# Kernel tuning notes

Hardware: AMD Instinct MI355X
Metric: run time of the kernel (lower is better)

The kernel has to match this reference:

```python
import jax, jax.numpy as jnp
import numpy as np

N, E, D, R = 100000, 1600000, 64, 16


def setup_inputs() -> dict:
    key = jax.random.key(0)
    k = jax.random.split(key, 8)
    feat = jax.random.normal(k[0], (N, D), dtype=jnp.float32)
    # xavier-uniform-ish scale (gain=sqrt(2), fan_in=fan_out=D) ~ std 0.177
    relation_weight = jax.random.normal(k[1], (R, D, D), dtype=jnp.float32) * 0.17
    relation_embed = jax.random.normal(k[2], (R, D), dtype=jnp.float32)
    W1 = jax.random.normal(k[3], (D, D), dtype=jnp.float32) * 0.1
    W2 = jax.random.normal(k[4], (D, D), dtype=jnp.float32) * 0.1
    src = jax.random.randint(k[5], (E,), 0, N, dtype=jnp.int32)
    dst = jax.random.randint(k[6], (E,), 0, N, dtype=jnp.int32)
    etype = jax.random.randint(k[7], (E,), 0, R, dtype=jnp.int32)
    return {"feat": feat, "relation_weight": relation_weight,
            "relation_embed": relation_embed, "W1": W1, "W2": W2,
            "src": src, "dst": dst, "etype": etype}


def reference(feat, relation_weight, relation_embed, W1, W2, src, dst, etype):
    n = feat.shape[0]
    # Project every node through every relation once ([N,R,D]) instead of
    # materializing the per-edge [E,D,D] weight gather; same math as
    # t_r = h_src @ W_{r(e)}, h_r = h_dst @ W_{r(e)}.
    proj = jnp.einsum('nd,rdo->nro', feat, relation_weight)  # [N,R,D]
    t_r = proj[src, etype]                                   # [E,D]
    h_r = proj[dst, etype]                                   # [E,D]
    # attention logit per edge: <t_r, tanh(h_r + r_embed)>
    att = jnp.sum(t_r * jnp.tanh(h_r + relation_embed[etype]), axis=-1)  # [E]
    # edge softmax over incoming edges of each destination node
    seg_max = jax.ops.segment_max(att, dst, num_segments=n)
    e = jnp.exp(att - seg_max[dst])
    seg_sum = jax.ops.segment_sum(e, dst, num_segments=n)
    a = e / seg_sum[dst]                                     # [E]
    # weighted aggregation of source features
    msgs = feat[src] * a[:, None]                            # [E,D]
    h_nb = jax.ops.segment_sum(msgs, dst, num_segments=n)    # [N,D]
    # Bi-interaction residual (torch leaky_relu default slope 0.01)
    out = (jax.nn.leaky_relu((feat + h_nb) @ W1.T, negative_slope=0.01)
           + jax.nn.leaky_relu((feat * h_nb) @ W2.T, negative_slope=0.01))
    return out
```

## Files before the change

kernel.cpp:

```cpp
#include <hip/hip_runtime.h>
#include <math.h>

#define D 64

typedef __attribute__((ext_vector_type(8))) short bf16x8;
typedef __attribute__((ext_vector_type(4))) float f32x4;

static __device__ __forceinline__ unsigned short f2bf(float f) {
    unsigned int u = __float_as_uint(f);
    unsigned int r = (u + 0x7FFFu + ((u >> 16) & 1u)) >> 16;
    return (unsigned short)r;
}
static __device__ __forceinline__ float bf2f(unsigned short h) {
    return __uint_as_float(((unsigned int)h) << 16);
}

#if defined(__has_builtin)
#if __has_builtin(__builtin_amdgcn_cvt_pk_bf16_f32)
#define HAVE_PK_BF16 1
#endif
#endif

static __device__ __forceinline__ unsigned int pk2bf(float a, float b) {
#ifdef HAVE_PK_BF16
    auto v = __builtin_amdgcn_cvt_pk_bf16_f32(a, b);
    return *(unsigned int*)&v;
#else
    return (unsigned int)f2bf(a) | ((unsigned int)f2bf(b) << 16);
#endif
}

static __device__ __forceinline__ float fast_tanh(float x) {
    float e = __expf(2.f * x);
    float r = __builtin_amdgcn_rcpf(e + 1.f);
    return 1.f - 2.f * r;
}

typedef __attribute__((address_space(1))) const unsigned int as1_uint;
typedef __attribute__((address_space(3))) unsigned int as3_uint;
static __device__ __forceinline__ void dma16(const void* g, void* l) {
    __builtin_amdgcn_global_load_lds((as1_uint*)g, (as3_uint*)l, 16, 0, 0);
}

__global__ __launch_bounds__(256) void k_wsplit(const float* __restrict__ W,
                                                unsigned short* __restrict__ B1h,
                                                unsigned short* __restrict__ B1l,
                                                unsigned short* __restrict__ B2h,
                                                unsigned short* __restrict__ B2l,
                                                int R) {
    int idx = blockIdx.x * 256 + threadIdx.x;
    int per_g = R * 512;
    if (idx >= 2 * per_g) return;
    int g = idx / per_g;
    int rest = idx % per_g;
    int r = rest >> 9;
    int rest2 = rest & 511;
    int c = rest2 >> 7;
    int kb = (rest2 >> 6) & 1;
    int lane = rest2 & 63;
    int m = lane & 15, q = lane >> 4;
    bf16x8 hv, lv;
    #pragma unroll
    for (int j = 0; j < 8; ++j) {
        float v;
        if (g == 0) v = W[(size_t)r * 4096 + (kb * 32 + q * 8 + j) * 64 + (c * 16 + m)];
        else        v = W[(size_t)r * 4096 + (c * 16 + m) * 64 + (kb * 32 + q * 8 + j)];
        unsigned short h = f2bf(v);
        hv[j] = (short)h;
        lv[j] = (short)f2bf(v - bf2f(h));
    }
    size_t off = ((((size_t)r * 4 + c) * 2 + kb) * 64 + lane) * 8;
    unsigned short* ph = (g == 0) ? B1h : B2h;
    unsigned short* pl = (g == 0) ? B1l : B2l;
    *(bf16x8*)&ph[off] = hv;
    *(bf16x8*)&pl[off] = lv;
}

__global__ __launch_bounds__(256) void k_wsplit2(const float* __restrict__ W1,
                                                 const float* __restrict__ W2,
                                                 unsigned short* __restrict__ F1h,
                                                 unsigned short* __restrict__ F1l,
                                                 unsigned short* __restrict__ F2h,
                                                 unsigned short* __restrict__ F2l) {
    int idx = blockIdx.x * 256 + threadIdx.x;
    if (idx >= 1024) return;
    int g = idx >> 9;
    int rest2 = idx & 511;
    int c = rest2 >> 7;
    int kb = (rest2 >> 6) & 1;
    int lane = rest2 & 63;
    int m = lane & 15, q = lane >> 4;
    const float* W = g ? W2 : W1;
    bf16x8 hv, lv;
    #pragma unroll
    for (int j = 0; j < 8; ++j) {
        float v = W[(c * 16 + m) * 64 + kb * 32 + q * 8 + j];
        unsigned short h = f2bf(v);
        hv[j] = (short)h;
        lv[j] = (short)f2bf(v - bf2f(h));
    }
    size_t off = (((size_t)c * 2 + kb) * 64 + lane) * 8;
    unsigned short* ph = g ? F2h : F1h;
    unsigned short* pl = g ? F2l : F1l;
    *(bf16x8*)&ph[off] = hv;
    *(bf16x8*)&pl[off] = lv;
}

#define NB3 256

__global__ __launch_bounds__(256) void k_bcount(const int* __restrict__ dst,
                                                int* __restrict__ cnt,
                                                int E, int CH, int NBUK) {
    __shared__ int h[1024];
    const int t = threadIdx.x, blk = blockIdx.x;
    for (int b = t; b < NBUK; b += 256) h[b] = 0;
    __syncthreads();
    const int s0 = blk * CH, s1 = min(E, s0 + CH);
    for (int e = s0 + t; e < s1; e += 256)
        atomicAdd(&h[dst[e] >> 7], 1);
    __syncthreads();
    for (int b = t; b < NBUK; b += 256)
        cnt[(b << 8) | blk] = h[b];
}

__global__ __launch_bounds__(256) void k_bscatter(const int* __restrict__ src,
                                                  const int* __restrict__ dst,
                                                  const int* __restrict__ etype,
                                                  const int* __restrict__ csc,
                                                  int* __restrict__ ebuf,
                                                  int E, int CH, int NBUK) {
    __shared__ int cur[1024];
    const int t = threadIdx.x, blk = blockIdx.x;
    for (int b = t; b < NBUK; b += 256) cur[b] = csc[(b << 8) | blk];
    __syncthreads();
    const int s0 = blk * CH, s1 = min(E, s0 + CH);
    for (int e = s0 + t; e < s1; e += 256) {
        int d = dst[e];
        int b = d >> 7;
        int pos = atomicAdd(&cur[b], 1);
        unsigned int pk = (unsigned int)src[e] | ((unsigned int)etype[e] << 20)
                        | ((unsigned int)(d & 127) << 25);
        ebuf[pos] = (int)pk;
    }
}

__global__ __launch_bounds__(256) void k_bcsr(const int* __restrict__ ebuf,
                                              const int* __restrict__ csc,
                                              int* __restrict__ offsets,
                                              int* __restrict__ spack,
                                              int N, int E, int NBUK) {
    __shared__ int sdeg[128], sincl[128], scur[128];
    const int t = threadIdx.x, b = blockIdx.x;
    const int s0 = csc[b << 8];
    const int s1 = csc[(b + 1) << 8];
    if (t < 128) { sdeg[t] = 0; }
    __syncthreads();
    for (int e = s0 + t; e < s1; e += 256)
        atomicAdd(&sdeg[((unsigned int)ebuf[e]) >> 25], 1);
    __syncthreads();
    if (t < 128) sincl[t] = sdeg[t];
    __syncthreads();
    for (int off = 1; off < 128; off <<= 1) {
        int v = 0;
        if (t < 128 && t >= off) v = sincl[t - off];
        __syncthreads();
        if (t < 128) sincl[t] += v;
        __syncthreads();
    }
    if (t < 128) {
        int excl = sincl[t] - sdeg[t];
        scur[t] = s0 + excl;
        int n = (b << 7) + t;
        if (n < N) offsets[n] = s0 + excl;
    }
    if (b == NBUK - 1 && t == 0) offsets[N] = E;
    __syncthreads();
    for (int e = s0 + t; e < s1; e += 256) {
        unsigned int pk = (unsigned int)ebuf[e];
        int i = pk >> 25;
        int p = atomicAdd(&scur[i], 1);
        spack[p] = (int)(pk & 0x01FFFFFFu);
    }
}

__global__ __launch_bounds__(1024) void k_scan1(const int* __restrict__ deg, int* __restrict__ tscan,
                                                int* __restrict__ bsum, int N) {
    __shared__ int s[1024];
    const int t = threadIdx.x;
    const int i = blockIdx.x * 1024 + t;
    int v = (i < N) ? deg[i] : 0;
    s[t] = v;
    __syncthreads();
    for (int off = 1; off < 1024; off <<= 1) {
        int tmp = (t >= off) ? s[t - off] : 0;
        __syncthreads();
        s[t] += tmp;
        __syncthreads();
    }
    if (i < N) tscan[i] = s[t];
    if (t == 1023) bsum[blockIdx.x] = s[1023];
}

__global__ __launch_bounds__(1024) void k_scan2(const int* __restrict__ bsum, int* __restrict__ bofs, int NB) {
    __shared__ int s[1024];
    const int t = threadIdx.x;
    int carry = 0;
    for (int b0 = 0; b0 < NB; b0 += 1024) {
        int i = b0 + t;
        int v = (i < NB) ? bsum[i] : 0;
        s[t] = v;
        __syncthreads();
        for (int off = 1; off < 1024; off <<= 1) {
            int tmp = (t >= off) ? s[t - off] : 0;
            __syncthreads();
            s[t] += tmp;
            __syncthreads();
        }
        if (i < NB) bofs[i] = carry + s[t] - v;
        int tot = s[1023];
        __syncthreads();
        carry += tot;
    }
}

__global__ __launch_bounds__(256) void k_scanout(const int* __restrict__ tscan, const int* __restrict__ bofs,
                                                 int* __restrict__ outv, int L) {
    int i = blockIdx.x * 256 + threadIdx.x;
    if (i <= L) {
        outv[i] = (i == 0) ? 0 : (tscan[i - 1] + bofs[(i - 1) >> 10]);
    }
}

__global__ __launch_bounds__(256, 4) void k_projv(const float* __restrict__ feat,
                                                  const unsigned short* __restrict__ B1h,
                                                  const unsigned short* __restrict__ B1l,
                                                  const unsigned short* __restrict__ B2h,
                                                  const unsigned short* __restrict__ B2l,
                                                  const float* __restrict__ emb,
                                                  unsigned short* __restrict__ V,
                                                  int N, int R, int nrq) {
    const int tile = blockIdx.x / nrq;
    const int rq   = blockIdx.x % nrq;
    const int rbase = rq * 4;
    const int rcnt  = (R - rbase < 4) ? (R - rbase) : 4;
    const int n0 = tile * 128;
    __shared__ __align__(16) unsigned short Bbuf[32][512];
    __shared__ __align__(16) unsigned short Us[4][1024];
    const int t = threadIdx.x;
    const int lane = t & 63, w = t >> 6;
    const int m = lane & 15, q = lane >> 4;

    bf16x8 ah[2][2], al[2][2];
    #pragma unroll
    for (int s = 0; s < 2; ++s) {
        int n = n0 + w * 32 + s * 16 + m;
        const float* rowp = feat + (size_t)n * D;
        #pragma unroll
        for (int kb = 0; kb < 2; ++kb) {
            int d0 = kb * 32 + q * 8;
            float4 v0 = make_float4(0.f, 0.f, 0.f, 0.f), v1 = v0;
            if (n < N) { v0 = *(const float4*)(rowp + d0); v1 = *(const float4*)(rowp + d0 + 4); }
            float vals[8] = {v0.x, v0.y, v0.z, v0.w, v1.x, v1.y, v1.z, v1.w};
            bf16x8 hv, lv;
            #pragma unroll
            for (int j = 0; j < 8; ++j) {
                unsigned short h = f2bf(vals[j]);
                hv[j] = (short)h;
                lv[j] = (short)f2bf(vals[j] - bf2f(h));
            }
            ah[s][kb] = hv; al[s][kb] = lv;
        }
    }

    auto stage_half = [&](int r, int half) {
        const unsigned short* arr = half ? ((w < 2) ? B2h : B2l)
                                         : ((w < 2) ? B1h : B1l);
        const unsigned short* gp = arr + (size_t)r * 4096 + (size_t)(w & 1) * 2048 + lane * 8;
        unsigned short* lp = &Bbuf[half * 16 + (w >> 1) * 8 + (w & 1) * 4][0];
        #pragma unroll
        for (int i = 0; i < 4; ++i)
            dma16(gp + i * 512, lp + i * 512);
    };

    stage_half(rbase, 0);
    stage_half(rbase, 1);
    __syncthreads();

    for (int rr = 0; rr < rcnt; ++rr) {
        const int r = rbase + rr;
        float em[4];
        #pragma unroll
        for (int c = 0; c < 4; ++c) em[c] = emb[r * 64 + c * 16 + m];

        f32x4 acc[4][2];
        #pragma unroll
        for (int c = 0; c < 4; ++c)
            #pragma unroll
            for (int s = 0; s < 2; ++s) acc[c][s] = (f32x4){0.f, 0.f, 0.f, 0.f};
        #pragma unroll
        for (int c = 0; c < 4; ++c) {
            bf16x8 bh[2], bl[2];
            #pragma unroll
            for (int kb = 0; kb < 2; ++kb) {
                bh[kb] = *(const bf16x8*)&Bbuf[c * 2 + kb][lane * 8];
                bl[kb] = *(const bf16x8*)&Bbuf[8 + c * 2 + kb][lane * 8];
            }
            #pragma unroll
            for (int s = 0; s < 2; ++s)
                #pragma unroll
                for (int kb = 0; kb < 2; ++kb) {
                    acc[c][s] = __builtin_amdgcn_mfma_f32_16x16x32_bf16(ah[s][kb], bh[kb], acc[c][s], 0, 0, 0);
                    acc[c][s] = __builtin_amdgcn_mfma_f32_16x16x32_bf16(al[s][kb], bh[kb], acc[c][s], 0, 0, 0);
                    acc[c][s] = __builtin_amdgcn_mfma_f32_16x16x32_bf16(ah[s][kb], bl[kb], acc[c][s], 0, 0, 0);
                }
        }

        __syncthreads();
        if (rr + 1 < rcnt) stage_half(r + 1, 0);

        #pragma unroll
        for (int s = 0; s < 2; ++s) {
            #pragma unroll
            for (int c = 0; c < 4; ++c) {
                int o = c * 16 + m;
                int kb2 = o >> 5;
                int q2 = (o >> 3) & 3;
                int j = o & 7;
                int Fb = kb2 * 64 + q2 * 16 + q * 4;
                #pragma unroll
                for (int i = 0; i < 4; i += 2) {
                    float t0 = fast_tanh(acc[c][s][i] + em[c]);
                    float t1 = fast_tanh(acc[c][s][i + 1] + em[c]);
                    unsigned int pk = pk2bf(t0, t1);
                    Us[w][((Fb + i) ^ q2) * 8 + j]     = (unsigned short)(pk & 0xFFFF);
                    Us[w][((Fb + i + 1) ^ q2) * 8 + j] = (unsigned short)(pk >> 16);
                }
            }

            bf16x8 ua[2];
            #pragma unroll
            for (int kb = 0; kb < 2; ++kb) {
                int F = kb * 64 + lane;
                ua[kb] = *(const bf16x8*)&Us[w][(F ^ (lane >> 4)) * 8];
            }
            f32x4 acc2[4];
            #pragma unroll
            for (int c = 0; c < 4; ++c) acc2[c] = (f32x4){0.f, 0.f, 0.f, 0.f};
            #pragma unroll
            for (int c = 0; c < 4; ++c) {
                bf16x8 bh[2], bl[2];
                #pragma unroll
                for (int kb = 0; kb < 2; ++kb) {
                    bh[kb] = *(const bf16x8*)&Bbuf[16 + c * 2 + kb][lane * 8];
                    bl[kb] = *(const bf16x8*)&Bbuf[24 + c * 2 + kb][lane * 8];
                }
                #pragma unroll
                for (int kb = 0; kb < 2; ++kb) {
                    acc2[c] = __builtin_amdgcn_mfma_f32_16x16x32_bf16(ua[kb], bh[kb], acc2[c], 0, 0, 0);
                    acc2[c] = __builtin_amdgcn_mfma_f32_16x16x32_bf16(ua[kb], bl[kb], acc2[c], 0, 0, 0);
                }
            }

            #pragma unroll
            for (int i = 0; i < 4; ++i) {
                int n = n0 + w * 32 + s * 16 + q * 4 + i;
                if (n < N) {
                    uint2 pv;
                    pv.x = pk2bf(acc2[0][i], acc2[1][i]);
                    pv.y = pk2bf(acc2[2][i], acc2[3][i]);
                    *(uint2*)&V[((size_t)n * R + r) * 64 + m * 4] = pv;
                }
            }
        }

        __syncthreads();
        if (rr + 1 < rcnt) stage_half(r + 1, 1);
    }
}

__global__ __launch_bounds__(256) void k_fused2(const unsigned short* __restrict__ V,
                                                const float* __restrict__ feat,
                                                const int* __restrict__ offsets,
                                                const int* __restrict__ spack,
                                                float* __restrict__ h_nb,
                                                int N, int R) {
    const int lane = threadIdx.x & 63;
    const int wav  = threadIdx.x >> 6;
    const int g    = lane >> 4;
    const int k    = lane & 15;
    const int n = blockIdx.x * 4 + wav;
    __shared__ float vlds[4][1024];
    if (n >= N) return;

    const unsigned int* v32 = (const unsigned int*)(V + (size_t)n * R * D);
    #pragma unroll
    for (int j = 0; j < 8; ++j) {
        int uidx = j * 64 + lane;
        unsigned int u = v32[uidx];
        int r  = uidx >> 5;
        int k2 = uidx & 31;
        int mm = k2 >> 1;
        int cc = (k2 & 1) * 2;
        int o  = cc * 16 + mm;
        vlds[wav][r * 64 + o]      = bf2f((unsigned short)(u & 0xFFFF));
        vlds[wav][r * 64 + o + 16] = bf2f((unsigned short)(u >> 16));
    }

    const int beg = offsets[n], end = offsets[n + 1];
    float m = -INFINITY, l = 0.f;
    float4 acc = make_float4(0.f, 0.f, 0.f, 0.f);

    if (beg < end) {
        int e = beg + g;
        bool ok = e < end;
        int pk = spack[ok ? e : (end - 1)];
        float4 f = *(const float4*)&feat[(size_t)(pk & 0xFFFFF) * D + k * 4];

        for (int i = beg; i < end; i += 4) {
            const int   et  = pk >> 20;
            const float4 fc = f;
            const bool  okc = ok;
            int e2 = i + 4 + g;
            ok = e2 < end;
            pk = spack[ok ? e2 : (end - 1)];
            f = *(const float4*)&feat[(size_t)(pk & 0xFFFFF) * D + k * 4];

            float4 v = *(const float4*)&vlds[wav][et * 64 + k * 4];
            float p = fc.x * v.x + fc.y * v.y + fc.z * v.z + fc.w * v.w;
            p += __shfl_xor(p, 1, 64);
            p += __shfl_xor(p, 2, 64);
            p += __shfl_xor(p, 4, 64);
            p += __shfl_xor(p, 8, 64);
            p = okc ? p : -INFINITY;
            float tmx = fmaxf(p, __shfl_xor(p, 16, 64));
            float nm4 = fmaxf(tmx, __shfl_xor(tmx, 32, 64));
            float nm  = fmaxf(m, nm4);
            float scale = __expf(m - nm);
            float wg    = __expf(p - nm);
            float sw = wg + __shfl_xor(wg, 16, 64);
            sw += __shfl_xor(sw, 32, 64);
            l = l * scale + sw;
            acc.x = acc.x * scale + wg * fc.x;
            acc.y = acc.y * scale + wg * fc.y;
            acc.z = acc.z * scale + wg * fc.z;
            acc.w = acc.w * scale + wg * fc.w;
            m = nm;
        }
        acc.x += __shfl_xor(acc.x, 16, 64);
        acc.y += __shfl_xor(acc.y, 16, 64);
        acc.z += __shfl_xor(acc.z, 16, 64);
        acc.w += __shfl_xor(acc.w, 16, 64);
        acc.x += __shfl_xor(acc.x, 32, 64);
        acc.y += __shfl_xor(acc.y, 32, 64);
        acc.z += __shfl_xor(acc.z, 32, 64);
        acc.w += __shfl_xor(acc.w, 32, 64);
        float inv = 1.f / l;
        acc.x *= inv; acc.y *= inv; acc.z *= inv; acc.w *= inv;
    }
    if (lane < 16)
        *(float4*)&h_nb[(size_t)n * D + k * 4] = acc;
}

__global__ __launch_bounds__(256, 2) void k_final(const float* __restrict__ feat,
                                                  const float* __restrict__ h_nb,
                                                  const unsigned short* __restrict__ F1h,
                                                  const unsigned short* __restrict__ F1l,
                                                  const unsigned short* __restrict__ F2h,
                                                  const unsigned short* __restrict__ F2l,
                                                  float* __restrict__ out, int N) {
    const int n0 = blockIdx.x * 128;
    __shared__ __align__(16) unsigned short Wlds[4][4096];
    const int t = threadIdx.x;
    const int lane = t & 63, w = t >> 6;
    const int m = lane & 15, q = lane >> 4;

    const unsigned short* warr = (w == 0) ? F1h : (w == 1) ? F1l : (w == 2) ? F2h : F2l;
    #pragma unroll
    for (int i = 0; i < 8; ++i)
        dma16(warr + i * 512 + lane * 8, &Wlds[w][i * 512]);

    bf16x8 sh[2][2], sl[2][2], ph[2][2], pl[2][2];
    #pragma unroll
    for (int s = 0; s < 2; ++s) {
        int n = n0 + w * 32 + s * 16 + m;
        const float* fp = feat + (size_t)n * D;
        const float* hp = h_nb + (size_t)n * D;
        #pragma unroll
        for (int kb = 0; kb < 2; ++kb) {
            int d0 = kb * 32 + q * 8;
            float4 f0 = make_float4(0.f, 0.f, 0.f, 0.f), f1 = f0, h0 = f0, h1 = f0;
            if (n < N) {
                f0 = *(const float4*)(fp + d0); f1 = *(const float4*)(fp + d0 + 4);
                h0 = *(const float4*)(hp + d0); h1 = *(const float4*)(hp + d0 + 4);
            }
            float fv[8] = {f0.x, f0.y, f0.z, f0.w, f1.x, f1.y, f1.z, f1.w};
            float hv[8] = {h0.x, h0.y, h0.z, h0.w, h1.x, h1.y, h1.z, h1.w};
            bf16x8 a, b, c2, d2;
            #pragma unroll
            for (int j = 0; j < 8; ++j) {
                float xs = fv[j] + hv[j];
                float xp = fv[j] * hv[j];
                unsigned short hs = f2bf(xs);
                unsigned short hp2 = f2bf(xp);
                a[j]  = (short)hs;
                b[j]  = (short)f2bf(xs - bf2f(hs));
                c2[j] = (short)hp2;
                d2[j] = (short)f2bf(xp - bf2f(hp2));
            }
            sh[s][kb] = a; sl[s][kb] = b; ph[s][kb] = c2; pl[s][kb] = d2;
        }
    }
    __syncthreads();

    f32x4 a1[4][2], a2[4][2];
    #pragma unroll
    for (int c = 0; c < 4; ++c)
        #pragma unroll
        for (int s = 0; s < 2; ++s) {
            a1[c][s] = (f32x4){0.f, 0.f, 0.f, 0.f};
            a2[c][s] = (f32x4){0.f, 0.f, 0.f, 0.f};
        }
    #pragma unroll
    for (int c = 0; c < 4; ++c) {
        bf16x8 b1h[2], b1l[2], b2h[2], b2l[2];
        #pragma unroll
        for (int kb = 0; kb < 2; ++kb) {
            int o = (c * 2 + kb) * 512 + lane * 8;
            b1h[kb] = *(const bf16x8*)&Wlds[0][o];
            b1l[kb] = *(const bf16x8*)&Wlds[1][o];
            b2h[kb] = *(const bf16x8*)&Wlds[2][o];
            b2l[kb] = *(const bf16x8*)&Wlds[3][o];
        }
        #pragma unroll
        for (int kb = 0; kb < 2; ++kb)
            #pragma unroll
            for (int s = 0; s < 2; ++s) {
                a1[c][s] = __builtin_amdgcn_mfma_f32_16x16x32_bf16(sh[s][kb], b1h[kb], a1[c][s], 0, 0, 0);
                a1[c][s] = __builtin_amdgcn_mfma_f32_16x16x32_bf16(sl[s][kb], b1h[kb], a1[c][s], 0, 0, 0);
                a1[c][s] = __builtin_amdgcn_mfma_f32_16x16x32_bf16(sh[s][kb], b1l[kb], a1[c][s], 0, 0, 0);
                a2[c][s] = __builtin_amdgcn_mfma_f32_16x16x32_bf16(ph[s][kb], b2h[kb], a2[c][s], 0, 0, 0);
                a2[c][s] = __builtin_amdgcn_mfma_f32_16x16x32_bf16(pl[s][kb], b2h[kb], a2[c][s], 0, 0, 0);
                a2[c][s] = __builtin_amdgcn_mfma_f32_16x16x32_bf16(ph[s][kb], b2l[kb], a2[c][s], 0, 0, 0);
            }
    }

    #pragma unroll
    for (int s = 0; s < 2; ++s)
        #pragma unroll
        for (int i = 0; i < 4; ++i) {
            int n = n0 + w * 32 + s * 16 + q * 4 + i;
            if (n < N) {
                #pragma unroll
                for (int c = 0; c < 4; ++c) {
                    float o1 = a1[c][s][i];
                    float o2 = a2[c][s][i];
                    o1 = (o1 > 0.f) ? o1 : 0.01f * o1;
                    o2 = (o2 > 0.f) ? o2 : 0.01f * o2;
                    out[(size_t)n * D + c * 16 + m] = o1 + o2;
                }
            }
        }
}

extern "C" void kernel_launch(void* const* d_in, const int* in_sizes, int n_in,
                              void* d_out, int out_size, void* d_ws, size_t ws_size,
                              hipStream_t stream) {
    const float* feat  = (const float*)d_in[0];
    const float* relW  = (const float*)d_in[1];
    const float* relE  = (const float*)d_in[2];
    const float* W1    = (const float*)d_in[3];
    const float* W2    = (const float*)d_in[4];
    const int*   src   = (const int*)d_in[5];
    const int*   dst   = (const int*)d_in[6];
    const int*   etype = (const int*)d_in[7];
    float* out = (float*)d_out;

    const int N = in_sizes[0] / D;
    const int R = in_sizes[2] / D;
    const int E = in_sizes[5];

    char* w = (char*)d_ws;
    size_t off = 0;
    auto alloc = [&](size_t bytes) -> void* {
        void* p = w + off;
        off = (off + bytes + 255) & ~(size_t)255;
        return p;
    };
    unsigned short* varr = (unsigned short*)alloc((size_t)N * R * D * sizeof(unsigned short));
    float* h_nb   = (float*)alloc((size_t)N * D * sizeof(float));
    int* offsets  = (int*)alloc((size_t)(N + 1) * sizeof(int));
    int* bsum     = (int*)alloc(2048 * sizeof(int));
    int* bofs     = (int*)alloc(2048 * sizeof(int));
    int* spack    = (int*)alloc((size_t)E * sizeof(int));
    size_t wfrag = (size_t)R * 4 * 2 * 64 * 8;
    unsigned short* B1h = (unsigned short*)alloc(wfrag * sizeof(unsigned short));
    unsigned short* B1l = (unsigned short*)alloc(wfrag * sizeof(unsigned short));
    unsigned short* B2h = (unsigned short*)alloc(wfrag * sizeof(unsigned short));
    unsigned short* B2l = (unsigned short*)alloc(wfrag * sizeof(unsigned short));
    unsigned short* F1h = (unsigned short*)alloc(4096 * sizeof(unsigned short));
    unsigned short* F1l = (unsigned short*)alloc(4096 * sizeof(unsigned short));
    unsigned short* F2h = (unsigned short*)alloc(4096 * sizeof(unsigned short));
    unsigned short* F2l = (unsigned short*)alloc(4096 * sizeof(unsigned short));
    (void)ws_size; (void)n_in; (void)out_size;

    const int NBUK = (N + 127) >> 7;
    const int CH   = (E + NB3 - 1) / NB3;
    const int L    = NBUK << 8;
    int* ebuf = (int*)varr;
    int* cnt  = ebuf + E;
    int* tsc  = cnt + L;
    int* csc  = tsc + L;
    const int NBscan = (L + 1023) / 1024;

    const int nrq = (R + 3) / 4;
    const int ntiles = (N + 127) / 128;

    k_wsplit<<<(2 * R * 512 + 255) / 256, 256, 0, stream>>>(relW, B1h, B1l, B2h, B2l, R);
    k_wsplit2<<<4, 256, 0, stream>>>(W1, W2, F1h, F1l, F2h, F2l);
    k_bcount<<<NB3, 256, 0, stream>>>(dst, cnt, E, CH, NBUK);
    k_scan1<<<NBscan, 1024, 0, stream>>>(cnt, tsc, bsum, L);
    k_scan2<<<1, 1024, 0, stream>>>(bsum, bofs, NBscan);
    k_scanout<<<(L + 1 + 255) / 256, 256, 0, stream>>>(tsc, bofs, csc, L);
    k_bscatter<<<NB3, 256, 0, stream>>>(src, dst, etype, csc, ebuf, E, CH, NBUK);
    k_bcsr<<<NBUK, 256, 0, stream>>>(ebuf, csc, offsets, spack, N, E, NBUK);
    k_projv<<<ntiles * nrq, 256, 0, stream>>>(feat, B1h, B1l, B2h, B2l, relE, varr, N, R, nrq);
    k_fused2<<<(N + 3) / 4, 256, 0, stream>>>(varr, feat, offsets, spack, h_nb, N, R);
    k_final<<<(N + 127) / 128, 256, 0, stream>>>(feat, h_nb, F1h, F1l, F2h, F2l, out, N);
}
```

Baseline: 369.1 us.

## Gather fp16 source features in edge kernel and merge small setup kernels

Adds a kernel that casts node features to fp16 once, and makes the fused edge kernel gather 8-byte fp16 rows instead of 16-byte fp32 rows. This halves the random-gather traffic over 1.6M edges. The two weight-split kernels are merged into one launch, and the scan-output kernel is removed: consumers now compute the exclusive-scan value inline from the tile scan and block offsets. The trade-offs are an extra pass over the features to cast them and fp16 rounding in the attention logits and messages.

```diff
diff --git a/kernel.cpp b/kernel.cpp
--- a/kernel.cpp
+++ b/kernel.cpp
@@ -42,68 +42,88 @@
     __builtin_amdgcn_global_load_lds((as1_uint*)g, (as3_uint*)l, 16, 0, 0);
 }
 
-__global__ __launch_bounds__(256) void k_wsplit(const float* __restrict__ W,
-                                                unsigned short* __restrict__ B1h,
-                                                unsigned short* __restrict__ B1l,
-                                                unsigned short* __restrict__ B2h,
-                                                unsigned short* __restrict__ B2l,
-                                                int R) {
-    int idx = blockIdx.x * 256 + threadIdx.x;
-    int per_g = R * 512;
-    if (idx >= 2 * per_g) return;
-    int g = idx / per_g;
-    int rest = idx % per_g;
-    int r = rest >> 9;
-    int rest2 = rest & 511;
-    int c = rest2 >> 7;
-    int kb = (rest2 >> 6) & 1;
-    int lane = rest2 & 63;
-    int m = lane & 15, q = lane >> 4;
-    bf16x8 hv, lv;
-    #pragma unroll
-    for (int j = 0; j < 8; ++j) {
-        float v;
-        if (g == 0) v = W[(size_t)r * 4096 + (kb * 32 + q * 8 + j) * 64 + (c * 16 + m)];
-        else        v = W[(size_t)r * 4096 + (c * 16 + m) * 64 + (kb * 32 + q * 8 + j)];
-        unsigned short h = f2bf(v);
-        hv[j] = (short)h;
-        lv[j] = (short)f2bf(v - bf2f(h));
-    }
-    size_t off = ((((size_t)r * 4 + c) * 2 + kb) * 64 + lane) * 8;
-    unsigned short* ph = (g == 0) ? B1h : B2h;
-    unsigned short* pl = (g == 0) ? B1l : B2l;
-    *(bf16x8*)&ph[off] = hv;
-    *(bf16x8*)&pl[off] = lv;
-}
-
-__global__ __launch_bounds__(256) void k_wsplit2(const float* __restrict__ W1,
+static __device__ __forceinline__ int exscan_at(const int* __restrict__ tsc,
+                                                const int* __restrict__ bofs, int i) {
+    return (i == 0) ? 0 : (tsc[i - 1] + bofs[(i - 1) >> 10]);
+}
+
+__global__ __launch_bounds__(256) void k_wsplitA(const float* __restrict__ W,
+                                                 unsigned short* __restrict__ B1h,
+                                                 unsigned short* __restrict__ B1l,
+                                                 unsigned short* __restrict__ B2h,
+                                                 unsigned short* __restrict__ B2l,
+                                                 const float* __restrict__ W1,
                                                  const float* __restrict__ W2,
                                                  unsigned short* __restrict__ F1h,
                                                  unsigned short* __restrict__ F1l,
                                                  unsigned short* __restrict__ F2h,
-                                                 unsigned short* __restrict__ F2l) {
+                                                 unsigned short* __restrict__ F2l,
+                                                 int R) {
     int idx = blockIdx.x * 256 + threadIdx.x;
-    if (idx >= 1024) return;
-    int g = idx >> 9;
-    int rest2 = idx & 511;
-    int c = rest2 >> 7;
-    int kb = (rest2 >> 6) & 1;
-    int lane = rest2 & 63;
-    int m = lane & 15, q = lane >> 4;
-    const float* W = g ? W2 : W1;
-    bf16x8 hv, lv;
-    #pragma unroll
-    for (int j = 0; j < 8; ++j) {
-        float v = W[(c * 16 + m) * 64 + kb * 32 + q * 8 + j];
-        unsigned short h = f2bf(v);
-        hv[j] = (short)h;
-        lv[j] = (short)f2bf(v - bf2f(h));
-    }
-    size_t off = (((size_t)c * 2 + kb) * 64 + lane) * 8;
-    unsigned short* ph = g ? F2h : F1h;
-    unsigned short* pl = g ? F2l : F1l;
-    *(bf16x8*)&ph[off] = hv;
-    *(bf16x8*)&pl[off] = lv;
+    int per_g = R * 512;
+    if (idx < 2 * per_g) {
+        int g = idx / per_g;
+        int rest = idx % per_g;
+        int r = rest >> 9;
+        int rest2 = rest & 511;
+        int c = rest2 >> 7;
+        int kb = (rest2 >> 6) & 1;
+        int lane = rest2 & 63;
+        int m = lane & 15, q = lane >> 4;
+        bf16x8 hv, lv;
+        #pragma unroll
+        for (int j = 0; j < 8; ++j) {
+            float v;
+            if (g == 0) v = W[(size_t)r * 4096 + (kb * 32 + q * 8 + j) * 64 + (c * 16 + m)];
+            else        v = W[(size_t)r * 4096 + (c * 16 + m) * 64 + (kb * 32 + q * 8 + j)];
+            unsigned short h = f2bf(v);
+            hv[j] = (short)h;
+            lv[j] = (short)f2bf(v - bf2f(h));
+        }
+        size_t off = ((((size_t)r * 4 + c) * 2 + kb) * 64 + lane) * 8;
+        unsigned short* ph = (g == 0) ? B1h : B2h;
+        unsigned short* pl = (g == 0) ? B1l : B2l;
+        *(bf16x8*)&ph[off] = hv;
+        *(bf16x8*)&pl[off] = lv;
+    } else {
+        int idx2 = idx - 2 * per_g;
+        if (idx2 >= 1024) return;
+        int g = idx2 >> 9;
+        int rest2 = idx2 & 511;
+        int c = rest2 >> 7;
+        int kb = (rest2 >> 6) & 1;
+        int lane = rest2 & 63;
+        int m = lane & 15, q = lane >> 4;
+        const float* Wx = g ? W2 : W1;
+        bf16x8 hv, lv;
+        #pragma unroll
+        for (int j = 0; j < 8; ++j) {
+            float v = Wx[(c * 16 + m) * 64 + kb * 32 + q * 8 + j];
+            unsigned short h = f2bf(v);
+            hv[j] = (short)h;
+            lv[j] = (short)f2bf(v - bf2f(h));
+        }
+        size_t off = (((size_t)c * 2 + kb) * 64 + lane) * 8;
+        unsigned short* ph = g ? F2h : F1h;
+        unsigned short* pl = g ? F2l : F1l;
+        *(bf16x8*)&ph[off] = hv;
+        *(bf16x8*)&pl[off] = lv;
+    }
+}
+
+__global__ __launch_bounds__(256) void k_fcast(const float* __restrict__ feat,
+                                               unsigned short* __restrict__ fb,
+                                               int total4) {
+    int i = blockIdx.x * 256 + threadIdx.x;
+    if (i < total4) {
+        float4 v = ((const float4*)feat)[i];
+        union { _Float16 h[4]; uint2 u; } cv;
+        cv.h[0] = (_Float16)v.x;
+        cv.h[1] = (_Float16)v.y;
+        cv.h[2] = (_Float16)v.z;
+        cv.h[3] = (_Float16)v.w;
+        ((uint2*)fb)[i] = cv.u;
+    }
 }
 
 #define NB3 256
@@ -126,12 +146,13 @@
 __global__ __launch_bounds__(256) void k_bscatter(const int* __restrict__ src,
                                                   const int* __restrict__ dst,
                                                   const int* __restrict__ etype,
-                                                  const int* __restrict__ csc,
+                                                  const int* __restrict__ tsc,
+                                                  const int* __restrict__ bofs,
                                                   int* __restrict__ ebuf,
                                                   int E, int CH, int NBUK) {
     __shared__ int cur[1024];
     const int t = threadIdx.x, blk = blockIdx.x;
-    for (int b = t; b < NBUK; b += 256) cur[b] = csc[(b << 8) | blk];
+    for (int b = t; b < NBUK; b += 256) cur[b] = exscan_at(tsc, bofs, (b << 8) | blk);
     __syncthreads();
     const int s0 = blk * CH, s1 = min(E, s0 + CH);
     for (int e = s0 + t; e < s1; e += 256) {
@@ -145,14 +166,15 @@
 }
 
 __global__ __launch_bounds__(256) void k_bcsr(const int* __restrict__ ebuf,
-                                              const int* __restrict__ csc,
+                                              const int* __restrict__ tsc,
+                                              const int* __restrict__ bofs,
                                               int* __restrict__ offsets,
                                               int* __restrict__ spack,
                                               int N, int E, int NBUK) {
     __shared__ int sdeg[128], sincl[128], scur[128];
     const int t = threadIdx.x, b = blockIdx.x;
-    const int s0 = csc[b << 8];
-    const int s1 = csc[(b + 1) << 8];
+    const int s0 = exscan_at(tsc, bofs, b << 8);
+    const int s1 = exscan_at(tsc, bofs, (b + 1) << 8);
     if (t < 128) { sdeg[t] = 0; }
     __syncthreads();
     for (int e = s0 + t; e < s1; e += 256)
@@ -220,14 +242,6 @@
         int tot = s[1023];
         __syncthreads();
         carry += tot;
-    }
-}
-
-__global__ __launch_bounds__(256) void k_scanout(const int* __restrict__ tscan, const int* __restrict__ bofs,
-                                                 int* __restrict__ outv, int L) {
-    int i = blockIdx.x * 256 + threadIdx.x;
-    if (i <= L) {
-        outv[i] = (i == 0) ? 0 : (tscan[i - 1] + bofs[(i - 1) >> 10]);
     }
 }
 
@@ -379,7 +393,7 @@
 }
 
 __global__ __launch_bounds__(256) void k_fused2(const unsigned short* __restrict__ V,
-                                                const float* __restrict__ feat,
+                                                const unsigned short* __restrict__ fb,
                                                 const int* __restrict__ offsets,
                                                 const int* __restrict__ spack,
                                                 float* __restrict__ h_nb,
@@ -414,16 +428,24 @@
         int e = beg + g;
         bool ok = e < end;
         int pk = spack[ok ? e : (end - 1)];
-        float4 f = *(const float4*)&feat[(size_t)(pk & 0xFFFFF) * D + k * 4];
+        uint2 fv = *(const uint2*)&fb[(size_t)(pk & 0xFFFFF) * D + k * 4];
 
         for (int i = beg; i < end; i += 4) {
             const int   et  = pk >> 20;
-            const float4 fc = f;
+            const uint2 fvc = fv;
             const bool  okc = ok;
             int e2 = i + 4 + g;
             ok = e2 < end;
             pk = spack[ok ? e2 : (end - 1)];
-            f = *(const float4*)&feat[(size_t)(pk & 0xFFFFF) * D + k * 4];
+            fv = *(const uint2*)&fb[(size_t)(pk & 0xFFFFF) * D + k * 4];
+
+            union { uint2 u; _Float16 h[4]; } cv;
+            cv.u = fvc;
+            float4 fc;
+            fc.x = (float)cv.h[0];
+            fc.y = (float)cv.h[1];
+            fc.z = (float)cv.h[2];
+            fc.w = (float)cv.h[3];
 
             float4 v = *(const float4*)&vlds[wav][et * 64 + k * 4];
             float p = fc.x * v.x + fc.y * v.y + fc.z * v.z + fc.w * v.w;
@@ -592,6 +614,7 @@
     int* bsum     = (int*)alloc(2048 * sizeof(int));
     int* bofs     = (int*)alloc(2048 * sizeof(int));
     int* spack    = (int*)alloc((size_t)E * sizeof(int));
+    unsigned short* fb = (unsigned short*)alloc((size_t)N * D * sizeof(unsigned short));
     size_t wfrag = (size_t)R * 4 * 2 * 64 * 8;
     unsigned short* B1h = (unsigned short*)alloc(wfrag * sizeof(unsigned short));
     unsigned short* B1l = (unsigned short*)alloc(wfrag * sizeof(unsigned short));
@@ -609,21 +632,21 @@
     int* ebuf = (int*)varr;
     int* cnt  = ebuf + E;
     int* tsc  = cnt + L;
-    int* csc  = tsc + L;
     const int NBscan = (L + 1023) / 1024;
 
     const int nrq = (R + 3) / 4;
     const int ntiles = (N + 127) / 128;
-
-    k_wsplit<<<(2 * R * 512 + 255) / 256, 256, 0, stream>>>(relW, B1h, B1l, B2h, B2l, R);
-    k_wsplit2<<<4, 256, 0, stream>>>(W1, W2, F1h, F1l, F2h, F2l);
+    const int nW = 2 * R * 512 + 1024;
+
+    k_wsplitA<<<(nW + 255) / 256, 256, 0, stream>>>(relW, B1h, B1l, B2h, B2l,
+                                                    W1, W2, F1h, F1l, F2h, F2l, R);
+    k_fcast<<<(N * D / 4 + 255) / 256, 256, 0, stream>>>(feat, fb, N * D / 4);
     k_bcount<<<NB3, 256, 0, stream>>>(dst, cnt, E, CH, NBUK);
     k_scan1<<<NBscan, 1024, 0, stream>>>(cnt, tsc, bsum, L);
     k_scan2<<<1, 1024, 0, stream>>>(bsum, bofs, NBscan);
-    k_scanout<<<(L + 1 + 255) / 256, 256, 0, stream>>>(tsc, bofs, csc, L);
-    k_bscatter<<<NB3, 256, 0, stream>>>(src, dst, etype, csc, ebuf, E, CH, NBUK);
-    k_bcsr<<<NBUK, 256, 0, stream>>>(ebuf, csc, offsets, spack, N, E, NBUK);
+    k_bscatter<<<NB3, 256, 0, stream>>>(src, dst, etype, tsc, bofs, ebuf, E, CH, NBUK);
+    k_bcsr<<<NBUK, 256, 0, stream>>>(ebuf, tsc, bofs, offsets, spack, N, E, NBUK);
     k_projv<<<ntiles * nrq, 256, 0, stream>>>(feat, B1h, B1l, B2h, B2l, relE, varr, N, R, nrq);
-    k_fused2<<<(N + 3) / 4, 256, 0, stream>>>(varr, feat, offsets, spack, h_nb, N, R);
+    k_fused2<<<(N + 3) / 4, 256, 0, stream>>>(varr, fb, offsets, spack, h_nb, N, R);
     k_final<<<(N + 127) / 128, 256, 0, stream>>>(feat, h_nb, F1h, F1l, F2h, F2l, out, N);
 }
```

Result: slower. 383.5 us (+3.9%).
